# Kernel tuning notes

Measured on AMD Instinct MI355X. Metric: run time of the kernel, lower is better.

## Reference

```python
import jax, jax.numpy as jnp
import numpy as np

NUM_HEADS = 8
TOP_K = 32
LN_EPS = 1e-5
RENORM_EPS = 1e-5


def _split_heads(x):
    # [B, S, D] -> [B, H, S, d]
    B, S, D = x.shape
    return x.reshape(B, S, NUM_HEADS, D // NUM_HEADS).transpose(0, 2, 1, 3)


def setup_inputs() -> dict:
    key = jax.random.key(0)
    k1, k2, k3, k4 = jax.random.split(key, 4)
    B, S, D, H = 2, 2048, 1024, NUM_HEADS
    q = jax.random.normal(k1, (B, S, D), dtype=jnp.float32)
    k = jax.random.normal(k2, (B, S, D), dtype=jnp.float32)
    v = jax.random.normal(k3, (B, S, D), dtype=jnp.float32)
    attention_weight = jax.random.normal(k4, (B, H, S, S), dtype=jnp.float32)
    gamma = jnp.ones((D,), dtype=jnp.float32)
    beta = jnp.zeros((D,), dtype=jnp.float32)
    return {"q": q, "k": k, "v": v, "attention_weight": attention_weight,
            "gamma": gamma, "beta": beta}


def reference(q, k, v, attention_weight, gamma, beta):
    B, S, D = q.shape
    qh = _split_heads(q)  # [B,H,S,d]
    kh = _split_heads(k)
    vh = _split_heads(v)
    # Unscaled QK^T (faithful to source: no /sqrt(d))
    scores = jnp.einsum("bhqd,bhkd->bhqk", qh, kh)
    probs = jax.nn.softmax(scores, axis=-1)
    # top-k mask via double argsort: rank of each key by descending weight
    rank = jnp.argsort(jnp.argsort(-attention_weight, axis=-1), axis=-1)
    top_mask = (rank < TOP_K).astype(probs.dtype)
    probs = probs * top_mask
    probs = probs / (jnp.sum(probs, axis=-1, keepdims=True) + RENORM_EPS)
    out = jnp.einsum("bhqk,bhkd->bhqd", probs, vh)
    out = out.transpose(0, 2, 1, 3).reshape(B, S, D)
    # LayerNorm over last dim
    mu = jnp.mean(out, axis=-1, keepdims=True)
    var = jnp.var(out, axis=-1, keepdims=True)
    out = (out - mu) * jax.lax.rsqrt(var + LN_EPS) * gamma + beta
    return out
```

## Files before the change

### kernel.cpp

```cpp
#include <hip/hip_runtime.h>
#include <stdint.h>

#define BB 2
#define SS 2048
#define DD 1024
#define HH 8
#define HD 128
#define TOPK 32
#define ROWS (BB*HH*SS)
#define BH 16

typedef float f32x4 __attribute__((ext_vector_type(4)));
typedef _Float16 f16x8 __attribute__((ext_vector_type(8)));
typedef _Float16 f16x4 __attribute__((ext_vector_type(4)));

__global__ __launch_bounds__(256) void cvt_kernel(const float* __restrict__ v,
                                                  _Float16* __restrict__ v16) {
    const int row = blockIdx.x;
    const int b = row >> 11, s = row & 2047;
    const int t = threadIdx.x;
    const int h = t >> 5, d4 = (t & 31) * 4;
    float4 f = *(const float4*)(v + (size_t)row * DD + t * 4);
    *(f16x4*)(v16 + ((size_t)(b * HH + h) * SS + s) * HD + d4) =
        (f16x4){(_Float16)f.x,(_Float16)f.y,(_Float16)f.z,(_Float16)f.w};
}

__global__ __launch_bounds__(256) void topk_kernel(const float* __restrict__ aw,
                                                   int* __restrict__ idx_out) {
    const int row = blockIdx.x;
    const float* p = aw + (size_t)row * SS;
    const int t = threadIdx.x;
    float4 v0 = *(const float4*)(p + 4 * t);
    float4 v1 = *(const float4*)(p + 1024 + 4 * t);
    float vals[8] = {v0.x, v0.y, v0.z, v0.w, v1.x, v1.y, v1.z, v1.w};
    unsigned long long key[8];
#pragma unroll
    for (int i = 0; i < 8; i++) {
        int e = (i < 4) ? (4 * t + i) : (1024 + 4 * t + (i - 4));
        unsigned u = __float_as_uint(vals[i]);
        unsigned sk = (u & 0x80000000u) ? ~u : (u | 0x80000000u);
        key[i] = ((unsigned long long)sk << 11) | (unsigned)(2047 - e);
    }
    __shared__ int s_cnt;
    __shared__ int s_red[4];
    __shared__ unsigned long long s_cand[256];
    const int lane = t & 63, wv = t >> 6;
    const unsigned long long lmask = (lane == 63) ? ~0ull >> 1 : (1ull << lane) - 1;

    unsigned thr0 = __float_as_uint(1.76f) | 0x80000000u;
    unsigned long long T = ((unsigned long long)thr0 << 11) | 2047ull;

    if (t == 0) s_cnt = 0;
    __syncthreads();
#pragma unroll
    for (int i = 0; i < 8; i++) {
        bool pred = key[i] > T;
        unsigned long long m = __ballot(pred);
        int base = 0;
        if (lane == 0 && m) base = atomicAdd(&s_cnt, __popcll(m));
        base = __shfl(base, 0, 64);
        if (pred) {
            int pos = base + __popcll(m & lmask);
            if (pos < 256) s_cand[pos] = key[i];
        }
    }
    __syncthreads();

    if (s_cnt < TOPK || s_cnt > 256) {
        unsigned long long lo = 0, hi = ~0ull;
        if (s_cnt > 256) lo = T; else hi = T;
        T = lo + ((hi - lo) >> 1);
        for (int it = 0; it < 40; ++it) {
            int c = 0;
#pragma unroll
            for (int i = 0; i < 8; i++) c += (key[i] > T) ? 1 : 0;
            for (int off = 32; off; off >>= 1) c += __shfl_down(c, off, 64);
            if (lane == 0) s_red[wv] = c;
            __syncthreads();
            int tot = s_red[0] + s_red[1] + s_red[2] + s_red[3];
            if (tot >= TOPK && tot <= 256) break;
            if (tot > 256) lo = T; else hi = T;
            T = lo + ((hi - lo) >> 1);
            __syncthreads();
        }
        if (t == 0) s_cnt = 0;
        __syncthreads();
#pragma unroll
        for (int i = 0; i < 8; i++) {
            bool pred = key[i] > T;
            unsigned long long m = __ballot(pred);
            int base = 0;
            if (lane == 0 && m) base = atomicAdd(&s_cnt, __popcll(m));
            base = __shfl(base, 0, 64);
            if (pred) {
                int pos = base + __popcll(m & lmask);
                if (pos < 256) s_cand[pos] = key[i];
            }
        }
        __syncthreads();
    }

    const int C = s_cnt < 256 ? s_cnt : 256;
    if (t < C) {
        unsigned long long mk = s_cand[t];
        int rank = 0;
        for (int j = 0; j < C; ++j)
            rank += (s_cand[j] > mk) ? 1 : 0;
        if (rank < TOPK)
            idx_out[(size_t)row * TOPK + rank] = 2047 - (int)(mk & 2047ull);
    }
}

__global__ __launch_bounds__(256) void stats_kernel(const float* __restrict__ q,
                                                    const float* __restrict__ k,
                                                    float* __restrict__ ws_m,
                                                    float* __restrict__ ws_l) {
    __shared__ __align__(16) _Float16 Ks[2][64 * 128];
    const int bid = blockIdx.x;
    const int t = threadIdx.x;
    const int xcd = bid & 7;
    const int r = bid >> 3;
    const int bh = xcd * 2 + (r & 1);
    const int rr = r >> 1;
    const int qt = rr & 15;
    const int quarter = rr >> 4;
    const int b = bh >> 3, h = bh & 7;
    const int wv = t >> 6, lane = t & 63;
    const int l16 = lane & 15, quad = lane >> 4;

    f16x8 af[2][4];
#pragma unroll
    for (int a = 0; a < 2; a++)
#pragma unroll
        for (int ks = 0; ks < 4; ks++) {
            const float* qs = q + (size_t)(b * SS + qt * 128 + wv * 32 + a * 16 + l16) * DD
                                + h * HD + ks * 32 + quad * 8;
            float4 f0 = *(const float4*)qs;
            float4 f1 = *(const float4*)(qs + 4);
            af[a][ks] = (f16x8){(_Float16)f0.x,(_Float16)f0.y,(_Float16)f0.z,(_Float16)f0.w,
                                (_Float16)f1.x,(_Float16)f1.y,(_Float16)f1.z,(_Float16)f1.w};
        }

    const int srow = t >> 2, cgrp = t & 3;
    const float* kb = k + (size_t)b * SS * DD + h * HD;

    int rdoff[4];
#pragma unroll
    for (int ks = 0; ks < 4; ks++)
        rdoff[ks] = (((ks * 4 + quad) ^ (l16 & 7)) * 8);

    float mrun[2][4], lrun[2][4];
#pragma unroll
    for (int a = 0; a < 2; a++)
#pragma unroll
        for (int r2 = 0; r2 < 4; r2++) { mrun[a][r2] = -INFINITY; lrun[a][r2] = 0.f; }

    {
        const float* src = kb + (size_t)(quarter * 8 * 64 + srow) * DD;
        float4 fr[8];
#pragma unroll
        for (int c = 0; c < 4; c++) {
            int cc = cgrp * 4 + c;
            fr[c * 2]     = *(const float4*)(src + cc * 8);
            fr[c * 2 + 1] = *(const float4*)(src + cc * 8 + 4);
        }
#pragma unroll
        for (int c = 0; c < 4; c++) {
            int cc = cgrp * 4 + c;
            f16x8 w = {(_Float16)fr[c*2].x,(_Float16)fr[c*2].y,(_Float16)fr[c*2].z,(_Float16)fr[c*2].w,
                       (_Float16)fr[c*2+1].x,(_Float16)fr[c*2+1].y,(_Float16)fr[c*2+1].z,(_Float16)fr[c*2+1].w};
            *(f16x8*)&Ks[0][srow * 128 + ((cc ^ (srow & 7)) * 8)] = w;
        }
    }
    __syncthreads();

    int cur = 0;
    for (int tt = 0; tt < 8; ++tt) {
        float4 nf[8];
        if (tt < 7) {
            const float* src = kb + (size_t)((quarter * 8 + tt + 1) * 64 + srow) * DD;
#pragma unroll
            for (int c = 0; c < 4; c++) {
                int cc = cgrp * 4 + c;
                nf[c * 2]     = *(const float4*)(src + cc * 8);
                nf[c * 2 + 1] = *(const float4*)(src + cc * 8 + 4);
            }
        }
        f32x4 acc[2][4];
#pragma unroll
        for (int a = 0; a < 2; a++)
#pragma unroll
            for (int n = 0; n < 4; n++) acc[a][n] = (f32x4){0.f, 0.f, 0.f, 0.f};
#pragma unroll
        for (int ks = 0; ks < 4; ++ks) {
            f16x8 bfr[4];
#pragma unroll
            for (int n = 0; n < 4; n++)
                bfr[n] = *(const f16x8*)&Ks[cur][(n * 16 + l16) * 128 + rdoff[ks]];
#pragma unroll
            for (int a = 0; a < 2; a++)
#pragma unroll
                for (int n = 0; n < 4; n++)
                    acc[a][n] = __builtin_amdgcn_mfma_f32_16x16x32_f16(af[a][ks], bfr[n], acc[a][n], 0, 0, 0);
        }
#pragma unroll
        for (int a = 0; a < 2; a++) {
#pragma unroll
            for (int r2 = 0; r2 < 4; r2++) {
                float tm = fmaxf(fmaxf(acc[a][0][r2], acc[a][1][r2]),
                                 fmaxf(acc[a][2][r2], acc[a][3][r2]));
#pragma unroll
                for (int off = 1; off < 16; off <<= 1) tm = fmaxf(tm, __shfl_xor(tm, off, 64));
                float tl = 0.f;
#pragma unroll
                for (int n = 0; n < 4; n++) tl += __expf(acc[a][n][r2] - tm);
#pragma unroll
                for (int off = 1; off < 16; off <<= 1) tl += __shfl_xor(tl, off, 64);
                float mo = mrun[a][r2];
                float mn = fmaxf(mo, tm);
                lrun[a][r2] = lrun[a][r2] * __expf(mo - mn) + tl * __expf(tm - mn);
                mrun[a][r2] = mn;
            }
        }
        if (tt < 7) {
#pragma unroll
            for (int c = 0; c < 4; c++) {
                int cc = cgrp * 4 + c;
                f16x8 w = {(_Float16)nf[c*2].x,(_Float16)nf[c*2].y,(_Float16)nf[c*2].z,(_Float16)nf[c*2].w,
                           (_Float16)nf[c*2+1].x,(_Float16)nf[c*2+1].y,(_Float16)nf[c*2+1].z,(_Float16)nf[c*2+1].w};
                *(f16x8*)&Ks[cur ^ 1][srow * 128 + ((cc ^ (srow & 7)) * 8)] = w;
            }
        }
        __syncthreads();
        cur ^= 1;
    }

    if (l16 == 0) {
#pragma unroll
        for (int a = 0; a < 2; a++)
#pragma unroll
            for (int r2 = 0; r2 < 4; r2++) {
                int rrow = qt * 128 + wv * 32 + a * 16 + quad * 4 + r2;
                size_t g = (size_t)quarter * ROWS + (size_t)bh * SS + rrow;
                ws_m[g] = mrun[a][r2];
                ws_l[g] = lrun[a][r2];
            }
    }
}

__global__ __launch_bounds__(128) void attnout_kernel(const float* __restrict__ q,
                                                      const float* __restrict__ k,
                                                      const _Float16* __restrict__ v16,
                                                      const int* __restrict__ idx_ws,
                                                      const float* __restrict__ ws_m,
                                                      const float* __restrict__ ws_l,
                                                      float* __restrict__ out) {
    const int bh = blockIdx.x & 15;
    const int s = blockIdx.x >> 4;
    const int R = (bh << 11) | s;
    const int b = bh >> 3, h = bh & 7;
    const int t = threadIdx.x;
    __shared__ float q_l[128];
    __shared__ int idx_l[32];
    __shared__ float e_l[32];
    __shared__ float w_l[32];
    __shared__ __align__(16) float s_pv[4][128];
    const float* qrow = q + ((size_t)(b * SS + s) * DD + h * HD);
    q_l[t] = qrow[t];
    if (t < 32) idx_l[t] = idx_ws[(size_t)R * TOPK + t];
    __syncthreads();
    float m = ws_m[R];
    m = fmaxf(m, ws_m[(size_t)ROWS + R]);
    m = fmaxf(m, ws_m[2 * (size_t)ROWS + R]);
    m = fmaxf(m, ws_m[3 * (size_t)ROWS + R]);
    float Z = 0.f;
#pragma unroll
    for (int qr = 0; qr < 4; ++qr)
        Z += ws_l[(size_t)qr * ROWS + R] * __expf(ws_m[(size_t)qr * ROWS + R] - m);

    const int l32 = t & 31, g = t >> 5;
    float4 q4 = *(const float4*)&q_l[l32 * 4];
    const float* kb = k + ((size_t)b * SS * DD + h * HD);
#pragma unroll
    for (int p = 0; p < 8; ++p) {
        int i = p * 4 + g;
        int ki = idx_l[i];
        float4 kv = *(const float4*)(kb + (size_t)ki * DD + l32 * 4);
        float d = q4.x * kv.x + q4.y * kv.y + q4.z * kv.z + q4.w * kv.w;
#pragma unroll
        for (int off = 1; off < 32; off <<= 1) d += __shfl_xor(d, off, 64);
        if (l32 == 0) e_l[i] = __expf(d - m);
    }
    __syncthreads();
    if (t < 32) {
        float e = e_l[t];
        float ssum = e;
#pragma unroll
        for (int off = 1; off < 32; off <<= 1) ssum += __shfl_xor(ssum, off, 64);
        float den = ssum + 1e-5f * Z;
        w_l[t] = e / den;
    }
    __syncthreads();
    const _Float16* vb = v16 + (size_t)bh * SS * HD;
    float a0 = 0.f, a1 = 0.f, a2 = 0.f, a3 = 0.f;
#pragma unroll
    for (int p = 0; p < 8; ++p) {
        int i = p * 4 + g;
        f16x4 hv = *(const f16x4*)(vb + (size_t)idx_l[i] * HD + l32 * 4);
        float w = w_l[i];
        a0 += w * (float)hv[0];
        a1 += w * (float)hv[1];
        a2 += w * (float)hv[2];
        a3 += w * (float)hv[3];
    }
    *(float4*)&s_pv[g][l32 * 4] = make_float4(a0, a1, a2, a3);
    __syncthreads();
    out[((size_t)(b * SS + s) * DD) + h * HD + t] =
        s_pv[0][t] + s_pv[1][t] + s_pv[2][t] + s_pv[3][t];
}

__global__ __launch_bounds__(256) void ln_kernel(float* __restrict__ out,
                                                 const float* __restrict__ gamma,
                                                 const float* __restrict__ beta) {
    const int row = blockIdx.x;
    float* p = out + (size_t)row * DD;
    const int t = threadIdx.x;
    float x[4];
#pragma unroll
    for (int i = 0; i < 4; i++) x[i] = p[t + 256 * i];
    float sum = x[0] + x[1] + x[2] + x[3];
    __shared__ float red[4];
    const int lane = t & 63, wv = t >> 6;
    for (int off = 32; off; off >>= 1) sum += __shfl_down(sum, off, 64);
    if (lane == 0) red[wv] = sum;
    __syncthreads();
    float mean = (red[0] + red[1] + red[2] + red[3]) * (1.f / DD);
    __syncthreads();
    float vs = 0.f;
#pragma unroll
    for (int i = 0; i < 4; i++) { float d = x[i] - mean; vs += d * d; }
    for (int off = 32; off; off >>= 1) vs += __shfl_down(vs, off, 64);
    if (lane == 0) red[wv] = vs;
    __syncthreads();
    float var = (red[0] + red[1] + red[2] + red[3]) * (1.f / DD);
    float inv = rsqrtf(var + 1e-5f);
#pragma unroll
    for (int i = 0; i < 4; i++) {
        int c = t + 256 * i;
        p[c] = (x[i] - mean) * inv * gamma[c] + beta[c];
    }
}

extern "C" void kernel_launch(void* const* d_in, const int* in_sizes, int n_in,
                              void* d_out, int out_size, void* d_ws, size_t ws_size,
                              hipStream_t stream) {
    const float* q = (const float*)d_in[0];
    const float* k = (const float*)d_in[1];
    const float* v = (const float*)d_in[2];
    const float* aw = (const float*)d_in[3];
    const float* gamma = (const float*)d_in[4];
    const float* beta = (const float*)d_in[5];
    float* out = (float*)d_out;

    int* idx_ws = (int*)d_ws;
    float* ws_m = (float*)((char*)d_ws + ((size_t)4 << 20));
    float* ws_l = ws_m + (size_t)4 * ROWS;
    _Float16* v16 = (_Float16*)((char*)d_ws + ((size_t)8 << 20));

    hipLaunchKernelGGL(cvt_kernel, dim3(BB * SS), dim3(256), 0, stream, v, v16);
    hipLaunchKernelGGL(topk_kernel, dim3(ROWS), dim3(256), 0, stream, aw, idx_ws);
    hipLaunchKernelGGL(stats_kernel, dim3(1024), dim3(256), 0, stream, q, k, ws_m, ws_l);
    hipLaunchKernelGGL(attnout_kernel, dim3(ROWS), dim3(128), 0, stream,
                       q, k, v16, idx_ws, ws_m, ws_l, out);
    hipLaunchKernelGGL(ln_kernel, dim3(BB * SS), dim3(256), 0, stream, out, gamma, beta);
}
```

Before: 528.0 us.

## Fuse conversion into top-k launch and attention output with LayerNorm

```diff
diff --git a/kernel.cpp b/kernel.cpp
--- a/kernel.cpp
+++ b/kernel.cpp
@@ -9,27 +9,40 @@
 #define TOPK 32
 #define ROWS (BB*HH*SS)
 #define BH 16
+#define NCVT (BB*SS)
 
 typedef float f32x4 __attribute__((ext_vector_type(4)));
 typedef _Float16 f16x8 __attribute__((ext_vector_type(8)));
 typedef _Float16 f16x4 __attribute__((ext_vector_type(4)));
 
-__global__ __launch_bounds__(256) void cvt_kernel(const float* __restrict__ v,
-                                                  _Float16* __restrict__ v16) {
-    const int row = blockIdx.x;
-    const int b = row >> 11, s = row & 2047;
+__global__ __launch_bounds__(256) void topk_cvt_kernel(const float* __restrict__ aw,
+                                                       const float* __restrict__ k,
+                                                       const float* __restrict__ v,
+                                                       _Float16* __restrict__ k16,
+                                                       _Float16* __restrict__ v16,
+                                                       int* __restrict__ idx_out) {
+    __shared__ int s_cnt;
+    __shared__ int s_red[4];
+    __shared__ unsigned long long s_cand[256];
+    const int bid = blockIdx.x;
     const int t = threadIdx.x;
-    const int h = t >> 5, d4 = (t & 31) * 4;
-    float4 f = *(const float4*)(v + (size_t)row * DD + t * 4);
-    *(f16x4*)(v16 + ((size_t)(b * HH + h) * SS + s) * HD + d4) =
-        (f16x4){(_Float16)f.x,(_Float16)f.y,(_Float16)f.z,(_Float16)f.w};
-}
-
-__global__ __launch_bounds__(256) void topk_kernel(const float* __restrict__ aw,
-                                                   int* __restrict__ idx_out) {
-    const int row = blockIdx.x;
+
+    if (bid < NCVT) {
+        const int row = bid;
+        const int b = row >> 11, s = row & 2047;
+        const int h = t >> 5, d4 = (t & 31) * 4;
+        const size_t src = (size_t)row * DD + t * 4;
+        const size_t dst = ((size_t)(b * HH + h) * SS + s) * HD + d4;
+        float4 f;
+        f = *(const float4*)(k + src);
+        *(f16x4*)(k16 + dst) = (f16x4){(_Float16)f.x,(_Float16)f.y,(_Float16)f.z,(_Float16)f.w};
+        f = *(const float4*)(v + src);
+        *(f16x4*)(v16 + dst) = (f16x4){(_Float16)f.x,(_Float16)f.y,(_Float16)f.z,(_Float16)f.w};
+        return;
+    }
+
+    const int row = bid - NCVT;
     const float* p = aw + (size_t)row * SS;
-    const int t = threadIdx.x;
     float4 v0 = *(const float4*)(p + 4 * t);
     float4 v1 = *(const float4*)(p + 1024 + 4 * t);
     float vals[8] = {v0.x, v0.y, v0.z, v0.w, v1.x, v1.y, v1.z, v1.w};
@@ -41,9 +54,6 @@
         unsigned sk = (u & 0x80000000u) ? ~u : (u | 0x80000000u);
         key[i] = ((unsigned long long)sk << 11) | (unsigned)(2047 - e);
     }
-    __shared__ int s_cnt;
-    __shared__ int s_red[4];
-    __shared__ unsigned long long s_cand[256];
     const int lane = t & 63, wv = t >> 6;
     const unsigned long long lmask = (lane == 63) ? ~0ull >> 1 : (1ull << lane) - 1;
 
@@ -248,88 +258,90 @@
     }
 }
 
-__global__ __launch_bounds__(128) void attnout_kernel(const float* __restrict__ q,
-                                                      const float* __restrict__ k,
-                                                      const _Float16* __restrict__ v16,
-                                                      const int* __restrict__ idx_ws,
-                                                      const float* __restrict__ ws_m,
-                                                      const float* __restrict__ ws_l,
-                                                      float* __restrict__ out) {
-    const int bh = blockIdx.x & 15;
-    const int s = blockIdx.x >> 4;
+__global__ __launch_bounds__(256) void attnout_ln_kernel(const float* __restrict__ q,
+                                                         const _Float16* __restrict__ k16,
+                                                         const _Float16* __restrict__ v16,
+                                                         const int* __restrict__ idx_ws,
+                                                         const float* __restrict__ ws_m,
+                                                         const float* __restrict__ ws_l,
+                                                         const float* __restrict__ gamma,
+                                                         const float* __restrict__ beta,
+                                                         float* __restrict__ out) {
+    const int row = blockIdx.x;
+    const int b = row >> 11, s = row & 2047;
+    const int t = threadIdx.x;
+    const int h = t >> 5, l32 = t & 31;
+    const int bh = b * HH + h;
     const int R = (bh << 11) | s;
-    const int b = bh >> 3, h = bh & 7;
-    const int t = threadIdx.x;
-    __shared__ float q_l[128];
-    __shared__ int idx_l[32];
-    __shared__ float e_l[32];
-    __shared__ float w_l[32];
-    __shared__ __align__(16) float s_pv[4][128];
-    const float* qrow = q + ((size_t)(b * SS + s) * DD + h * HD);
-    q_l[t] = qrow[t];
-    if (t < 32) idx_l[t] = idx_ws[(size_t)R * TOPK + t];
-    __syncthreads();
-    float m = ws_m[R];
-    m = fmaxf(m, ws_m[(size_t)ROWS + R]);
-    m = fmaxf(m, ws_m[2 * (size_t)ROWS + R]);
-    m = fmaxf(m, ws_m[3 * (size_t)ROWS + R]);
-    float Z = 0.f;
-#pragma unroll
-    for (int qr = 0; qr < 4; ++qr)
-        Z += ws_l[(size_t)qr * ROWS + R] * __expf(ws_m[(size_t)qr * ROWS + R] - m);
-
-    const int l32 = t & 31, g = t >> 5;
-    float4 q4 = *(const float4*)&q_l[l32 * 4];
-    const float* kb = k + ((size_t)b * SS * DD + h * HD);
-#pragma unroll
-    for (int p = 0; p < 8; ++p) {
-        int i = p * 4 + g;
-        int ki = idx_l[i];
-        float4 kv = *(const float4*)(kb + (size_t)ki * DD + l32 * 4);
-        float d = q4.x * kv.x + q4.y * kv.y + q4.z * kv.z + q4.w * kv.w;
+
+    __shared__ __align__(16) float q_l[1024];
+    __shared__ int   idx_l[8][32];
+    __shared__ float e_l[8][32];
+    __shared__ float w_l[8][32];
+    __shared__ float mZ_l[8][2];
+    __shared__ __align__(16) float o_l[1024];
+    __shared__ float red[4];
+
+    *(float4*)&q_l[t * 4] = *(const float4*)(q + (size_t)row * DD + t * 4);
+    idx_l[h][l32] = idx_ws[(size_t)R * TOPK + l32];
+    if (t < 8) {
+        int Rh = ((b * HH + t) << 11) | s;
+        float m = ws_m[Rh];
+        m = fmaxf(m, ws_m[(size_t)ROWS + Rh]);
+        m = fmaxf(m, ws_m[2 * (size_t)ROWS + Rh]);
+        m = fmaxf(m, ws_m[3 * (size_t)ROWS + Rh]);
+        float Z = 0.f;
+#pragma unroll
+        for (int qr = 0; qr < 4; ++qr)
+            Z += ws_l[(size_t)qr * ROWS + Rh] * __expf(ws_m[(size_t)qr * ROWS + Rh] - m);
+        mZ_l[t][0] = m;
+        mZ_l[t][1] = Z;
+    }
+    __syncthreads();
+
+    const _Float16* kbh = k16 + (size_t)bh * SS * HD;
+    float4 q4 = *(const float4*)&q_l[h * HD + l32 * 4];
+    const float m = mZ_l[h][0];
+#pragma unroll 8
+    for (int i = 0; i < 32; ++i) {
+        int ki = idx_l[h][i];
+        f16x4 kv = *(const f16x4*)(kbh + (size_t)ki * HD + l32 * 4);
+        float d = q4.x * (float)kv[0] + q4.y * (float)kv[1]
+                + q4.z * (float)kv[2] + q4.w * (float)kv[3];
 #pragma unroll
         for (int off = 1; off < 32; off <<= 1) d += __shfl_xor(d, off, 64);
-        if (l32 == 0) e_l[i] = __expf(d - m);
-    }
-    __syncthreads();
-    if (t < 32) {
-        float e = e_l[t];
+        if (l32 == 0) e_l[h][i] = __expf(d - m);
+    }
+    __syncthreads();
+
+    {
+        float e = e_l[h][l32];
         float ssum = e;
 #pragma unroll
         for (int off = 1; off < 32; off <<= 1) ssum += __shfl_xor(ssum, off, 64);
-        float den = ssum + 1e-5f * Z;
-        w_l[t] = e / den;
-    }
-    __syncthreads();
-    const _Float16* vb = v16 + (size_t)bh * SS * HD;
+        float den = ssum + 1e-5f * mZ_l[h][1];
+        w_l[h][l32] = e / den;
+    }
+    __syncthreads();
+
+    const _Float16* vbh = v16 + (size_t)bh * SS * HD;
     float a0 = 0.f, a1 = 0.f, a2 = 0.f, a3 = 0.f;
-#pragma unroll
-    for (int p = 0; p < 8; ++p) {
-        int i = p * 4 + g;
-        f16x4 hv = *(const f16x4*)(vb + (size_t)idx_l[i] * HD + l32 * 4);
-        float w = w_l[i];
+#pragma unroll 8
+    for (int i = 0; i < 32; ++i) {
+        f16x4 hv = *(const f16x4*)(vbh + (size_t)idx_l[h][i] * HD + l32 * 4);
+        float w = w_l[h][i];
         a0 += w * (float)hv[0];
         a1 += w * (float)hv[1];
         a2 += w * (float)hv[2];
         a3 += w * (float)hv[3];
     }
-    *(float4*)&s_pv[g][l32 * 4] = make_float4(a0, a1, a2, a3);
-    __syncthreads();
-    out[((size_t)(b * SS + s) * DD) + h * HD + t] =
-        s_pv[0][t] + s_pv[1][t] + s_pv[2][t] + s_pv[3][t];
-}
-
-__global__ __launch_bounds__(256) void ln_kernel(float* __restrict__ out,
-                                                 const float* __restrict__ gamma,
-                                                 const float* __restrict__ beta) {
-    const int row = blockIdx.x;
-    float* p = out + (size_t)row * DD;
-    const int t = threadIdx.x;
+    *(float4*)&o_l[h * HD + l32 * 4] = make_float4(a0, a1, a2, a3);
+    __syncthreads();
+
     float x[4];
 #pragma unroll
-    for (int i = 0; i < 4; i++) x[i] = p[t + 256 * i];
+    for (int i = 0; i < 4; i++) x[i] = o_l[t + 256 * i];
     float sum = x[0] + x[1] + x[2] + x[3];
-    __shared__ float red[4];
     const int lane = t & 63, wv = t >> 6;
     for (int off = 32; off; off >>= 1) sum += __shfl_down(sum, off, 64);
     if (lane == 0) red[wv] = sum;
@@ -347,7 +359,7 @@
 #pragma unroll
     for (int i = 0; i < 4; i++) {
         int c = t + 256 * i;
-        p[c] = (x[i] - mean) * inv * gamma[c] + beta[c];
+        out[(size_t)row * DD + c] = (x[i] - mean) * inv * gamma[c] + beta[c];
     }
 }
 
@@ -365,12 +377,12 @@
     int* idx_ws = (int*)d_ws;
     float* ws_m = (float*)((char*)d_ws + ((size_t)4 << 20));
     float* ws_l = ws_m + (size_t)4 * ROWS;
-    _Float16* v16 = (_Float16*)((char*)d_ws + ((size_t)8 << 20));
-
-    hipLaunchKernelGGL(cvt_kernel, dim3(BB * SS), dim3(256), 0, stream, v, v16);
-    hipLaunchKernelGGL(topk_kernel, dim3(ROWS), dim3(256), 0, stream, aw, idx_ws);
+    _Float16* k16 = (_Float16*)((char*)d_ws + ((size_t)8 << 20));
+    _Float16* v16 = k16 + (size_t)BH * SS * HD;
+
+    hipLaunchKernelGGL(topk_cvt_kernel, dim3(NCVT + ROWS), dim3(256), 0, stream,
+                       aw, k, v, k16, v16, idx_ws);
     hipLaunchKernelGGL(stats_kernel, dim3(1024), dim3(256), 0, stream, q, k, ws_m, ws_l);
-    hipLaunchKernelGGL(attnout_kernel, dim3(ROWS), dim3(128), 0, stream,
-                       q, k, v16, idx_ws, ws_m, ws_l, out);
-    hipLaunchKernelGGL(ln_kernel, dim3(BB * SS), dim3(256), 0, stream, out, gamma, beta);
+    hipLaunchKernelGGL(attnout_ln_kernel, dim3(NCVT), dim3(256), 0, stream,
+                       q, k16, v16, idx_ws, ws_m, ws_l, gamma, beta, out);
 }
```

Measured after the change: 532.0 us. About the same (+0.8%).
